# Kernel tuning notes

Hardware: AMD Instinct MI355X
Metric: run time of the kernel (lower is better)

## Reference

```python
import jax, jax.numpy as jnp
import numpy as np

EMBED_VOCAB = 16 * 1024 * 1024
EPS = 1e-5


def setup_inputs() -> dict:
    key = jax.random.key(0)
    ks = jax.random.split(key, 16)
    B = 65536
    state = jax.random.randint(ks[0], (B,), 0, 4, dtype=jnp.int32)
    counts = jax.random.randint(ks[1], (B,), 0, 200, dtype=jnp.int32)
    mp = jax.random.randint(ks[2], (B, 7, 7), 0, EMBED_VOCAB, dtype=jnp.int32)
    # learned parameters
    embed_table = jax.random.normal(ks[3], (EMBED_VOCAB, 8), dtype=jnp.float32)
    state_table = jax.random.normal(ks[4], (4, 32), dtype=jnp.float32)
    counts_table = jax.random.normal(ks[5], (200, 16), dtype=jnp.float32)
    d_in = 8 * 49 + 32 + 16  # 440
    W1 = jax.random.normal(ks[6], (256, d_in), dtype=jnp.float32) * (1.0 / np.sqrt(d_in))
    b1 = jnp.zeros((256,), dtype=jnp.float32)
    gamma = jnp.ones((256,), dtype=jnp.float32)
    beta = jnp.zeros((256,), dtype=jnp.float32)
    W2 = jax.random.normal(ks[7], (64, 256), dtype=jnp.float32) * (1.0 / np.sqrt(256))
    b2 = jnp.zeros((64,), dtype=jnp.float32)
    W3 = jax.random.normal(ks[8], (16, 64), dtype=jnp.float32) * (1.0 / np.sqrt(64))
    b3 = jnp.zeros((16,), dtype=jnp.float32)
    W4 = jax.random.normal(ks[9], (1, 16), dtype=jnp.float32) * 0.25
    b4 = jnp.zeros((1,), dtype=jnp.float32)
    return {
        "state": state, "counts": counts, "mp": mp,
        "embed_table": embed_table, "state_table": state_table, "counts_table": counts_table,
        "W1": W1, "b1": b1, "gamma": gamma, "beta": beta,
        "W2": W2, "b2": b2, "W3": W3, "b3": b3, "W4": W4, "b4": b4,
    }


def reference(state, counts, mp, embed_table, state_table, counts_table,
              W1, b1, gamma, beta, W2, b2, W3, b3, W4, b4):
    B = mp.shape[0]
    # gather embeddings
    x = embed_table[jnp.remainder(mp, EMBED_VOCAB)]      # [B,7,7,8]
    x = x.reshape(B, 49 * 8)                              # flatten dims 1..2 then last
    s = state_table[state]                                # [B,32]
    c = counts_table[counts]                              # [B,16]
    h = jnp.concatenate((s, c, x), axis=1)                # [B,440]
    # Linear 440->256
    h = h @ W1.T + b1
    # BatchNorm1d(256), training mode (batch statistics, biased variance)
    mu = jnp.mean(h, axis=0)
    var = jnp.mean((h - mu) ** 2, axis=0)
    h = (h - mu) * jax.lax.rsqrt(var + EPS) * gamma + beta
    # Linear 256->64 + ReLU
    h = jax.nn.relu(h @ W2.T + b2)
    # Linear 64->16 + ReLU
    h = jax.nn.relu(h @ W3.T + b3)
    # Linear 16->1
    out = h @ W4.T + b4                                   # [B,1]
    return out.reshape(B)
```

## Files before the change

### kernel.cpp

```cpp
#include <hip/hip_runtime.h>

typedef __attribute__((ext_vector_type(4))) float f32x4;
typedef __attribute__((ext_vector_type(8))) short bfrag;

#define NCH 256
#define BN_EPS 1e-5f

__device__ __forceinline__ unsigned short cvt_bf16(float f){
  unsigned u = __float_as_uint(f);
  u += 0x7FFFu + ((u >> 16) & 1u);
  return (unsigned short)(u >> 16);
}
__device__ __forceinline__ float bf16tof(unsigned short h){
  return __uint_as_float(((unsigned)h) << 16);
}
__device__ __forceinline__ void split2(const f32x4 va, const f32x4 vb, bfrag& hi, bfrag& lo){
  #pragma unroll
  for (int e = 0; e < 4; ++e){
    unsigned short h0 = cvt_bf16(va[e]);
    hi[e]   = (short)h0;
    lo[e]   = (short)cvt_bf16(va[e] - bf16tof(h0));
    unsigned short h1b = cvt_bf16(vb[e]);
    hi[4+e] = (short)h1b;
    lo[4+e] = (short)cvt_bf16(vb[e] - bf16tof(h1b));
  }
}

#define GLOAD_LDS16(gp, lp) \
  __builtin_amdgcn_global_load_lds((const __attribute__((address_space(1))) unsigned*)(gp), \
                                   (__attribute__((address_space(3))) unsigned*)(lp), 16, 0, 0)

__global__ void k_prep(const float* __restrict__ W1, const float* __restrict__ W2,
                       unsigned short* __restrict__ W1p, unsigned short* __restrict__ W2p,
                       float* __restrict__ gsum){
  int t = blockIdx.x * 256 + threadIdx.x;
  if (t < 14 * 8192){
    int e = t & 7, l = (t >> 3) & 63, c = (t >> 9) & 15, s = t >> 13;
    int chan = c * 16 + (l & 15);
    int k = s * 32 + (l >> 4) * 8 + e;
    float v = (k < 440) ? W1[chan * 440 + k] : 0.f;
    W1p[s * 8192 + c * 512 + l * 8 + e] = cvt_bf16(v);
  }
  if (t < 16384){
    int e = t & 7, l = (t >> 3) & 63, c = (t >> 9) & 3, s = t >> 11;
    int chan = c * 16 + (l & 15);
    int k = s * 32 + (l >> 4) * 8 + e;
    W2p[s * 2048 + c * 512 + l * 8 + e] = cvt_bf16(W2[chan * 256 + k]);
  }
  if (t < 512) gsum[t] = 0.f;
}

__device__ __forceinline__ void stage_w(const char* __restrict__ wsrc, char* smem,
                                        int S, int BUF, int w, int l){
  #pragma unroll
  for (int r = 0; r < 4; ++r)
    GLOAD_LDS16(wsrc + S * 16384 + (w * 4 + r) * 1024 + l * 16,
                smem + BUF * 16384 + (w * 4 + r) * 1024);
}

__global__ __launch_bounds__(256, 2) void k_gemm1(
    const int* __restrict__ state, const int* __restrict__ counts, const int* __restrict__ mp,
    const float* __restrict__ embed, const float* __restrict__ stab, const float* __restrict__ ctab,
    const unsigned short* __restrict__ W1p, const float* __restrict__ b1,
    unsigned short* __restrict__ h1b, float* __restrict__ gsum)
{
  __shared__ __align__(16) char smem[2 * 16384];
  __shared__ __align__(16) int  mp_lds[6272];
  __shared__ float wsum[4][256];
  __shared__ float wsq[4][256];

  const int tid = threadIdx.x;
  const int w  = tid >> 6;
  const int l  = tid & 63;
  const int lr = l & 15;
  const int g  = l >> 4;
  const int rowbase = blockIdx.x * 128 + w * 32;
  const int arow0 = rowbase + lr;
  const int arow1 = rowbase + 16 + lr;

  const int st0 = state[arow0] * 32, st1 = state[arow1] * 32;
  const int ct0 = counts[arow0] * 16, ct1 = counts[arow1] * 16;
  const char* wsrc = (const char*)W1p;

  {
    const char* mpsrc = (const char*)(mp + (size_t)blockIdx.x * 6272);
    #pragma unroll
    for (int it = 0; it < 7; ++it){
      int idx = it * 256 + tid;
      if (idx < 1568)
        GLOAD_LDS16(mpsrc + idx * 16, (char*)mp_lds + idx * 16);
    }
  }

  f32x4 xva[3][2], xvb[3][2];
  f32x4 acc0[16], acc1[16];
  #pragma unroll
  for (int i = 0; i < 16; ++i){ acc0[i] = (f32x4){0.f,0.f,0.f,0.f}; acc1[i] = acc0[i]; }

  #define ISSUE_X(S) do {                                            \
    const float *p0_, *p1_;                                          \
    if ((S) == 0){ p0_ = stab + st0 + g * 8; p1_ = stab + st1 + g * 8; } \
    else if ((S) == 1 && g < 2){                                     \
      p0_ = ctab + ct0 + g * 8; p1_ = ctab + ct1 + g * 8;            \
    } else {                                                         \
      int m_ = 4 * (S) + g - 6;                                      \
      m_ = m_ < 0 ? 0 : (m_ > 48 ? 48 : m_);                         \
      p0_ = embed + ((mp_lds[(w * 32 + lr) * 49 + m_]      & 0xFFFFFF) << 3); \
      p1_ = embed + ((mp_lds[(w * 32 + 16 + lr) * 49 + m_] & 0xFFFFFF) << 3); \
    }                                                                \
    xva[(S)%3][0] = *(const f32x4*)p0_;  xvb[(S)%3][0] = *(const f32x4*)(p0_ + 4); \
    xva[(S)%3][1] = *(const f32x4*)p1_;  xvb[(S)%3][1] = *(const f32x4*)(p1_ + 4); \
  } while(0)

  stage_w(wsrc, smem, 0, 0, w, l);
  ISSUE_X(0);
  asm volatile("s_waitcnt vmcnt(0)" ::: "memory");
  __builtin_amdgcn_sched_barrier(0);
  __builtin_amdgcn_s_barrier();
  ISSUE_X(1);
  asm volatile("" ::: "memory");
  __builtin_amdgcn_sched_barrier(0);

  bfrag ahi0, alo0, ahi1, alo1;

  #pragma unroll
  for (int s = 0; s < 14; ++s){
    if (s < 13) stage_w(wsrc, smem, s + 1, (s + 1) & 1, w, l);
    asm volatile("" ::: "memory");
    __builtin_amdgcn_sched_barrier(0);

    {
      f32x4 va0 = xva[s % 3][0], vb0 = xvb[s % 3][0];
      f32x4 va1 = xva[s % 3][1], vb1 = xvb[s % 3][1];
      if (s == 13 && g == 3){
        va0 = (f32x4){0.f,0.f,0.f,0.f}; vb0 = va0; va1 = va0; vb1 = va0;
      }
      split2(va0, vb0, ahi0, alo0);
      split2(va1, vb1, ahi1, alo1);
    }
    if (s < 12) ISSUE_X(s + 2);

    __builtin_amdgcn_sched_barrier(0);
    if (s <= 11)      asm volatile("s_waitcnt vmcnt(12)" ::: "memory");
    else if (s == 12) asm volatile("s_waitcnt vmcnt(8)"  ::: "memory");
    else              asm volatile("s_waitcnt vmcnt(0)"  ::: "memory");
    __builtin_amdgcn_sched_barrier(0);
    __builtin_amdgcn_s_barrier();

    {
      const char* base = smem + (s & 1) * 16384 + l * 16;
      #pragma unroll
      for (int c = 0; c < 16; ++c){
        const bfrag bhi = *(const bfrag*)(base + c * 1024);
        acc0[c] = __builtin_amdgcn_mfma_f32_16x16x32_bf16(ahi0, bhi, acc0[c], 0, 0, 0);
        acc0[c] = __builtin_amdgcn_mfma_f32_16x16x32_bf16(alo0, bhi, acc0[c], 0, 0, 0);
        acc1[c] = __builtin_amdgcn_mfma_f32_16x16x32_bf16(ahi1, bhi, acc1[c], 0, 0, 0);
        acc1[c] = __builtin_amdgcn_mfma_f32_16x16x32_bf16(alo1, bhi, acc1[c], 0, 0, 0);
      }
    }

    __builtin_amdgcn_s_barrier();
  }
  #undef ISSUE_X

  #pragma unroll
  for (int c = 0; c < 16; ++c){
    const int j = c * 16 + lr;
    const float bb = b1[j];
    float s = 0.f, q = 0.f;
    #pragma unroll
    for (int e = 0; e < 4; ++e){
      float h = acc0[c][e] + bb;
      s += h; q += h * h;
      h1b[(rowbase + g * 4 + e) * NCH + j] = cvt_bf16(h);
    }
    #pragma unroll
    for (int e = 0; e < 4; ++e){
      float h = acc1[c][e] + bb;
      s += h; q += h * h;
      h1b[(rowbase + 16 + g * 4 + e) * NCH + j] = cvt_bf16(h);
    }
    s += __shfl_xor(s, 16);  s += __shfl_xor(s, 32);
    q += __shfl_xor(q, 16);  q += __shfl_xor(q, 32);
    if (g == 0){ wsum[w][j] = s; wsq[w][j] = q; }
  }
  __syncthreads();
  {
    float s = wsum[0][tid] + wsum[1][tid] + wsum[2][tid] + wsum[3][tid];
    float q = wsq[0][tid]  + wsq[1][tid]  + wsq[2][tid]  + wsq[3][tid];
    atomicAdd(&gsum[tid], s);
    atomicAdd(&gsum[256 + tid], q);
  }
}

__global__ __launch_bounds__(256, 3) void k_tail(
    const unsigned short* __restrict__ h1b, const float* __restrict__ gsum,
    const float* __restrict__ gamma, const float* __restrict__ beta,
    const unsigned short* __restrict__ W2p,
    const float* __restrict__ b2, const float* __restrict__ W3, const float* __restrict__ b3,
    const float* __restrict__ W4, const float* __restrict__ b4,
    float* __restrict__ out)
{
  __shared__ float ssl[512];
  __shared__ __align__(16) short w2s[16384];
  __shared__ float h2l[4][16][65];

  const int tid = threadIdx.x;
  const int w  = tid >> 6;
  const int l  = tid & 63;
  const int lr = l & 15;
  const int g  = l >> 4;
  const int rowbase = blockIdx.x * 128 + w * 32;

  {
    float su = gsum[tid];
    float sq = gsum[256 + tid];
    float mu  = su * (1.f / 65536.f);
    float var = sq * (1.f / 65536.f) - mu * mu;
    float sc  = gamma[tid] * rsqrtf(var + BN_EPS);
    ssl[tid]       = sc;
    ssl[256 + tid] = beta[tid] - mu * sc;
  }
  #pragma unroll
  for (int it = 0; it < 8; ++it)
    GLOAD_LDS16((const char*)W2p + (it * 256 + tid) * 16, (char*)w2s + (it * 256 + tid) * 16);
  __syncthreads();

  const float b4v = b4[0];

  #pragma unroll
  for (int t = 0; t < 2; ++t){
    const int rowt = rowbase + t * 16;

    f32x4 acc[4];
    #pragma unroll
    for (int i = 0; i < 4; ++i) acc[i] = (f32x4){0.f, 0.f, 0.f, 0.f};

    #pragma unroll
    for (int s = 0; s < 8; ++s){
      const int kk = s * 32 + g * 8;
      bfrag hv = *(const bfrag*)(h1b + (rowt + lr) * 256 + kk);
      bfrag ahi, alo;
      #pragma unroll
      for (int e = 0; e < 8; ++e){
        float x = fmaf(bf16tof((unsigned short)hv[e]), ssl[kk + e], ssl[256 + kk + e]);
        unsigned short h0 = cvt_bf16(x);
        ahi[e] = (short)h0;
        alo[e] = (short)cvt_bf16(x - bf16tof(h0));
      }
      const char* base = (const char*)w2s + s * 4096 + l * 16;
      #pragma unroll
      for (int c = 0; c < 4; ++c){
        const bfrag bhi = *(const bfrag*)(base + c * 1024);
        acc[c] = __builtin_amdgcn_mfma_f32_16x16x32_bf16(ahi, bhi, acc[c], 0, 0, 0);
        acc[c] = __builtin_amdgcn_mfma_f32_16x16x32_bf16(alo, bhi, acc[c], 0, 0, 0);
      }
    }

    #pragma unroll
    for (int c = 0; c < 4; ++c){
      int j = c * 16 + lr;
      float bb = b2[j];
      #pragma unroll
      for (int e = 0; e < 4; ++e){
        float h = acc[c][e] + bb;
        h2l[w][g * 4 + e][j] = h > 0.f ? h : 0.f;
      }
    }

    float a3[4];
    #pragma unroll
    for (int t3 = 0; t3 < 4; ++t3) a3[t3] = b3[g * 4 + t3];
    #pragma unroll 4
    for (int k = 0; k < 64; ++k){
      float hv = h2l[w][lr][k];
      #pragma unroll
      for (int t3 = 0; t3 < 4; ++t3) a3[t3] += hv * W3[(g * 4 + t3) * 64 + k];
    }

    float p = 0.f;
    #pragma unroll
    for (int t3 = 0; t3 < 4; ++t3){
      float h = a3[t3] > 0.f ? a3[t3] : 0.f;
      p += h * W4[g * 4 + t3];
    }
    p += __shfl_xor(p, 16);
    p += __shfl_xor(p, 32);
    if (l < 16) out[rowt + lr] = p + b4v;
  }
}

extern "C" void kernel_launch(void* const* d_in, const int* in_sizes, int n_in,
                              void* d_out, int out_size, void* d_ws, size_t ws_size,
                              hipStream_t stream){
  const int*   state = (const int*)d_in[0];
  const int*   counts= (const int*)d_in[1];
  const int*   mp    = (const int*)d_in[2];
  const float* embed = (const float*)d_in[3];
  const float* stab  = (const float*)d_in[4];
  const float* ctab  = (const float*)d_in[5];
  const float* W1    = (const float*)d_in[6];
  const float* b1    = (const float*)d_in[7];
  const float* gamma = (const float*)d_in[8];
  const float* beta  = (const float*)d_in[9];
  const float* W2    = (const float*)d_in[10];
  const float* b2    = (const float*)d_in[11];
  const float* W3    = (const float*)d_in[12];
  const float* b3    = (const float*)d_in[13];
  const float* W4    = (const float*)d_in[14];
  const float* b4    = (const float*)d_in[15];
  float* out = (float*)d_out;

  char* ws = (char*)d_ws;
  unsigned short* h1bf = (unsigned short*)(ws);
  float* gsum          = (float*)(ws + 33554432);
  unsigned short* W1p  = (unsigned short*)(ws + 33558528);
  unsigned short* W2p  = (unsigned short*)(ws + 33787904);

  k_prep <<<448, 256, 0, stream>>>(W1, W2, W1p, W2p, gsum);
  k_gemm1<<<512, 256, 0, stream>>>(state, counts, mp, embed, stab, ctab,
                                   W1p, b1, h1bf, gsum);
  k_tail <<<512, 256, 0, stream>>>(h1bf, gsum, gamma, beta, W2p,
                                   b2, W3, b3, W4, b4, out);
}
```

Before: 117.4 us.

## Warp-specialize gemm1: producer waves gather and split embeddings into LDS for MFMA waves

Each gemm1 block now has 512 threads. Four producer waves gather the state, counts and embedding rows, split them into bf16 hi/lo pairs, and write them to a double-buffered, XOR-swizzled LDS area. Four consumer waves stage W1 and run the MFMAs on the A fragments read from LDS. The mp indices are read straight from global instead of being staged in LDS. The per-block stat reduction in LDS is replaced with per-wave atomics to gsum. The aim is to overlap random gather latency with the matrix work, at the cost of 64KB of LDS per block, more atomics, and a reliance on the barrier count matching between the two roles.

```diff
diff --git a/kernel.cpp b/kernel.cpp
--- a/kernel.cpp
+++ b/kernel.cpp
@@ -58,97 +58,117 @@
                 smem + BUF * 16384 + (w * 4 + r) * 1024);
 }
 
-__global__ __launch_bounds__(256, 2) void k_gemm1(
+__global__ __launch_bounds__(512, 2) void k_gemm1(
     const int* __restrict__ state, const int* __restrict__ counts, const int* __restrict__ mp,
     const float* __restrict__ embed, const float* __restrict__ stab, const float* __restrict__ ctab,
     const unsigned short* __restrict__ W1p, const float* __restrict__ b1,
     unsigned short* __restrict__ h1b, float* __restrict__ gsum)
 {
-  __shared__ __align__(16) char smem[2 * 16384];
-  __shared__ __align__(16) int  mp_lds[6272];
-  __shared__ float wsum[4][256];
-  __shared__ float wsq[4][256];
+  __shared__ __align__(16) char lds[65536];
 
   const int tid = threadIdx.x;
   const int w  = tid >> 6;
   const int l  = tid & 63;
-  const int lr = l & 15;
-  const int g  = l >> 4;
-  const int rowbase = blockIdx.x * 128 + w * 32;
-  const int arow0 = rowbase + lr;
-  const int arow1 = rowbase + 16 + lr;
-
-  const int st0 = state[arow0] * 32, st1 = state[arow1] * 32;
-  const int ct0 = counts[arow0] * 16, ct1 = counts[arow1] * 16;
   const char* wsrc = (const char*)W1p;
 
-  {
-    const char* mpsrc = (const char*)(mp + (size_t)blockIdx.x * 6272);
-    #pragma unroll
-    for (int it = 0; it < 7; ++it){
-      int idx = it * 256 + tid;
-      if (idx < 1568)
-        GLOAD_LDS16(mpsrc + idx * 16, (char*)mp_lds + idx * 16);
-    }
-  }
-
-  f32x4 xva[3][2], xvb[3][2];
-  f32x4 acc0[16], acc1[16];
-  #pragma unroll
-  for (int i = 0; i < 16; ++i){ acc0[i] = (f32x4){0.f,0.f,0.f,0.f}; acc1[i] = acc0[i]; }
-
-  #define ISSUE_X(S) do {                                            \
-    const float *p0_, *p1_;                                          \
-    if ((S) == 0){ p0_ = stab + st0 + g * 8; p1_ = stab + st1 + g * 8; } \
-    else if ((S) == 1 && g < 2){                                     \
-      p0_ = ctab + ct0 + g * 8; p1_ = ctab + ct1 + g * 8;            \
-    } else {                                                         \
-      int m_ = 4 * (S) + g - 6;                                      \
-      m_ = m_ < 0 ? 0 : (m_ > 48 ? 48 : m_);                         \
-      p0_ = embed + ((mp_lds[(w * 32 + lr) * 49 + m_]      & 0xFFFFFF) << 3); \
-      p1_ = embed + ((mp_lds[(w * 32 + 16 + lr) * 49 + m_] & 0xFFFFFF) << 3); \
-    }                                                                \
-    xva[(S)%3][0] = *(const f32x4*)p0_;  xvb[(S)%3][0] = *(const f32x4*)(p0_ + 4); \
-    xva[(S)%3][1] = *(const f32x4*)p1_;  xvb[(S)%3][1] = *(const f32x4*)(p1_ + 4); \
-  } while(0)
-
-  stage_w(wsrc, smem, 0, 0, w, l);
-  ISSUE_X(0);
-  asm volatile("s_waitcnt vmcnt(0)" ::: "memory");
-  __builtin_amdgcn_sched_barrier(0);
-  __builtin_amdgcn_s_barrier();
-  ISSUE_X(1);
-  asm volatile("" ::: "memory");
-  __builtin_amdgcn_sched_barrier(0);
-
-  bfrag ahi0, alo0, ahi1, alo1;
-
-  #pragma unroll
-  for (int s = 0; s < 14; ++s){
-    if (s < 13) stage_w(wsrc, smem, s + 1, (s + 1) & 1, w, l);
-    asm volatile("" ::: "memory");
-    __builtin_amdgcn_sched_barrier(0);
-
+  if (w >= 4){
+    const int q  = w - 4;
+    const int g  = l & 3;
+    const int rA = q * 32 + (l >> 2);
+    const int rB = rA + 16;
+    const int gA = blockIdx.x * 128 + rA;
+    const int gB = blockIdx.x * 128 + rB;
+
+    const int stA = state[gA] * 32,  stB = state[gB] * 32;
+    const int ctA = counts[gA] * 16, ctB = counts[gB] * 16;
+
+    int   mAv[14], mBv[14];
+    f32x4 pa[14][2], pb[14][2];
+
+    #define MCOL(S) ((S) == 1 ? (g >= 2 ? g - 2 : 0) \
+                              : (4*(S) + g - 6 > 48 ? 48 : 4*(S) + g - 6))
+
+    mAv[1] = mp[gA * 49 + MCOL(1)];  mBv[1] = mp[gB * 49 + MCOL(1)];
+    mAv[2] = mp[gA * 49 + MCOL(2)];  mBv[2] = mp[gB * 49 + MCOL(2)];
     {
-      f32x4 va0 = xva[s % 3][0], vb0 = xvb[s % 3][0];
-      f32x4 va1 = xva[s % 3][1], vb1 = xvb[s % 3][1];
-      if (s == 13 && g == 3){
-        va0 = (f32x4){0.f,0.f,0.f,0.f}; vb0 = va0; va1 = va0; vb1 = va0;
-      }
-      split2(va0, vb0, ahi0, alo0);
-      split2(va1, vb1, ahi1, alo1);
-    }
-    if (s < 12) ISSUE_X(s + 2);
-
-    __builtin_amdgcn_sched_barrier(0);
-    if (s <= 11)      asm volatile("s_waitcnt vmcnt(12)" ::: "memory");
-    else if (s == 12) asm volatile("s_waitcnt vmcnt(8)"  ::: "memory");
-    else              asm volatile("s_waitcnt vmcnt(0)"  ::: "memory");
-    __builtin_amdgcn_sched_barrier(0);
-    __builtin_amdgcn_s_barrier();
-
+      const float* aA = stab + stA + g * 8;
+      const float* aB = stab + stB + g * 8;
+      pa[0][0] = *(const f32x4*)aA; pb[0][0] = *(const f32x4*)(aA + 4);
+      pa[0][1] = *(const f32x4*)aB; pb[0][1] = *(const f32x4*)(aB + 4);
+    }
     {
-      const char* base = smem + (s & 1) * 16384 + l * 16;
+      const float* aA = (g < 2) ? (ctab + ctA + g * 8) : (embed + ((mAv[1] & 0xFFFFFF) << 3));
+      const float* aB = (g < 2) ? (ctab + ctB + g * 8) : (embed + ((mBv[1] & 0xFFFFFF) << 3));
+      pa[1][0] = *(const f32x4*)aA; pb[1][0] = *(const f32x4*)(aA + 4);
+      pa[1][1] = *(const f32x4*)aB; pb[1][1] = *(const f32x4*)(aB + 4);
+    }
+
+    #pragma unroll
+    for (int S = 0; S < 14; ++S){
+      if (S <= 10){
+        mAv[S+3] = mp[gA * 49 + MCOL(S+3)];
+        mBv[S+3] = mp[gB * 49 + MCOL(S+3)];
+      }
+      f32x4 a0 = pa[S][0], b0 = pb[S][0], a1 = pa[S][1], b1r = pb[S][1];
+      if (S == 13 && g == 3){
+        a0 = (f32x4){0.f,0.f,0.f,0.f}; b0 = a0; a1 = a0; b1r = a0;
+      }
+      bfrag hi0, lo0, hi1, lo1;
+      split2(a0, b0, hi0, lo0);
+      split2(a1, b1r, hi1, lo1);
+      {
+        char* slot = lds + 32768 + (S & 1) * 16384;
+        *(bfrag*)(slot + rA*128 + ((g*16)      ^ ((rA & 7) << 4))) = hi0;
+        *(bfrag*)(slot + rA*128 + ((64 + g*16) ^ ((rA & 7) << 4))) = lo0;
+        *(bfrag*)(slot + rB*128 + ((g*16)      ^ ((rB & 7) << 4))) = hi1;
+        *(bfrag*)(slot + rB*128 + ((64 + g*16) ^ ((rB & 7) << 4))) = lo1;
+      }
+      if (S <= 11){
+        const float* aA = embed + ((mAv[S+2] & 0xFFFFFF) << 3);
+        const float* aB = embed + ((mBv[S+2] & 0xFFFFFF) << 3);
+        pa[S+2][0] = *(const f32x4*)aA; pb[S+2][0] = *(const f32x4*)(aA + 4);
+        pa[S+2][1] = *(const f32x4*)aB; pb[S+2][1] = *(const f32x4*)(aB + 4);
+      }
+      __builtin_amdgcn_sched_barrier(0);
+      asm volatile("s_waitcnt lgkmcnt(0)" ::: "memory");
+      __builtin_amdgcn_sched_barrier(0);
+      __builtin_amdgcn_s_barrier();
+      __builtin_amdgcn_s_barrier();
+    }
+    #undef MCOL
+    return;
+
+  } else {
+    const int lr = l & 15;
+    const int g  = l >> 4;
+    const int rowbase = blockIdx.x * 128 + w * 32;
+    const int rl0 = w * 32 + lr, rl1 = rl0 + 16;
+
+    f32x4 acc0[16], acc1[16];
+    #pragma unroll
+    for (int i = 0; i < 16; ++i){ acc0[i] = (f32x4){0.f,0.f,0.f,0.f}; acc1[i] = acc0[i]; }
+
+    stage_w(wsrc, lds, 0, 0, w, l);
+
+    #pragma unroll
+    for (int S = 0; S < 14; ++S){
+      if (S < 13) stage_w(wsrc, lds, S + 1, (S + 1) & 1, w, l);
+
+      __builtin_amdgcn_sched_barrier(0);
+      if (S < 13) asm volatile("s_waitcnt vmcnt(4)" ::: "memory");
+      else        asm volatile("s_waitcnt vmcnt(0)" ::: "memory");
+      __builtin_amdgcn_sched_barrier(0);
+      __builtin_amdgcn_s_barrier();
+      asm volatile("" ::: "memory");
+      __builtin_amdgcn_sched_barrier(0);
+
+      const char* slot = lds + 32768 + (S & 1) * 16384;
+      const bfrag ahi0 = *(const bfrag*)(slot + rl0*128 + ((g*16)      ^ ((rl0 & 7) << 4)));
+      const bfrag alo0 = *(const bfrag*)(slot + rl0*128 + ((64 + g*16) ^ ((rl0 & 7) << 4)));
+      const bfrag ahi1 = *(const bfrag*)(slot + rl1*128 + ((g*16)      ^ ((rl1 & 7) << 4)));
+      const bfrag alo1 = *(const bfrag*)(slot + rl1*128 + ((64 + g*16) ^ ((rl1 & 7) << 4)));
+
+      const char* base = lds + (S & 1) * 16384 + l * 16;
       #pragma unroll
       for (int c = 0; c < 16; ++c){
         const bfrag bhi = *(const bfrag*)(base + c * 1024);
@@ -157,39 +177,33 @@
         acc1[c] = __builtin_amdgcn_mfma_f32_16x16x32_bf16(ahi1, bhi, acc1[c], 0, 0, 0);
         acc1[c] = __builtin_amdgcn_mfma_f32_16x16x32_bf16(alo1, bhi, acc1[c], 0, 0, 0);
       }
-    }
-
-    __builtin_amdgcn_s_barrier();
-  }
-  #undef ISSUE_X
-
-  #pragma unroll
-  for (int c = 0; c < 16; ++c){
-    const int j = c * 16 + lr;
-    const float bb = b1[j];
-    float s = 0.f, q = 0.f;
-    #pragma unroll
-    for (int e = 0; e < 4; ++e){
-      float h = acc0[c][e] + bb;
-      s += h; q += h * h;
-      h1b[(rowbase + g * 4 + e) * NCH + j] = cvt_bf16(h);
-    }
-    #pragma unroll
-    for (int e = 0; e < 4; ++e){
-      float h = acc1[c][e] + bb;
-      s += h; q += h * h;
-      h1b[(rowbase + 16 + g * 4 + e) * NCH + j] = cvt_bf16(h);
-    }
-    s += __shfl_xor(s, 16);  s += __shfl_xor(s, 32);
-    q += __shfl_xor(q, 16);  q += __shfl_xor(q, 32);
-    if (g == 0){ wsum[w][j] = s; wsq[w][j] = q; }
-  }
-  __syncthreads();
-  {
-    float s = wsum[0][tid] + wsum[1][tid] + wsum[2][tid] + wsum[3][tid];
-    float q = wsq[0][tid]  + wsq[1][tid]  + wsq[2][tid]  + wsq[3][tid];
-    atomicAdd(&gsum[tid], s);
-    atomicAdd(&gsum[256 + tid], q);
+      __builtin_amdgcn_s_barrier();
+    }
+
+    #pragma unroll
+    for (int c = 0; c < 16; ++c){
+      const int j = c * 16 + lr;
+      const float bb = b1[j];
+      float s = 0.f, qq = 0.f;
+      #pragma unroll
+      for (int e = 0; e < 4; ++e){
+        float h = acc0[c][e] + bb;
+        s += h; qq += h * h;
+        h1b[(rowbase + g * 4 + e) * NCH + j] = cvt_bf16(h);
+      }
+      #pragma unroll
+      for (int e = 0; e < 4; ++e){
+        float h = acc1[c][e] + bb;
+        s += h; qq += h * h;
+        h1b[(rowbase + 16 + g * 4 + e) * NCH + j] = cvt_bf16(h);
+      }
+      s  += __shfl_xor(s, 16);  s  += __shfl_xor(s, 32);
+      qq += __shfl_xor(qq, 16); qq += __shfl_xor(qq, 32);
+      if (g == 0){
+        atomicAdd(&gsum[j], s);
+        atomicAdd(&gsum[256 + j], qq);
+      }
+    }
   }
 }
 
@@ -318,7 +332,7 @@
   unsigned short* W2p  = (unsigned short*)(ws + 33787904);
 
   k_prep <<<448, 256, 0, stream>>>(W1, W2, W1p, W2p, gsum);
-  k_gemm1<<<512, 256, 0, stream>>>(state, counts, mp, embed, stab, ctab,
+  k_gemm1<<<512, 512, 0, stream>>>(state, counts, mp, embed, stab, ctab,
                                    W1p, b1, h1bf, gsum);
   k_tail <<<512, 256, 0, stream>>>(h1bf, gsum, gamma, beta, W2p,
                                    b2, W3, b3, W4, b4, out);
```

Measured after the change: 152.5 us. 1.3x slower.

## Fuse GEMM1 and tail via grid-wide barrier, keep activations in registers

Applied to the files above, without the earlier changes.

Merges the first GEMM and the BatchNorm/MLP tail into one persistent kernel. A global atomic counter acts as a grid barrier after the batch statistics are accumulated, so the 256-wide hidden activations stay in MFMA accumulators instead of being written to and re-read from a bf16 buffer in global memory. The MFMA operands are swapped so the accumulator layout feeds directly into the second GEMM's A fragments, and W2 is repacked to match. This removes a kernel launch and roughly 64 MB of HBM traffic plus bf16 rounding of h1. The cost is that all 512 blocks must be co-resident or the spin-wait deadlocks, and the barrier serialises the slowest block.

```diff
diff --git a/kernel.cpp b/kernel.cpp
--- a/kernel.cpp
+++ b/kernel.cpp
@@ -4,6 +4,7 @@
 typedef __attribute__((ext_vector_type(8))) short bfrag;
 
 #define NCH 256
+#define NBLK 512
 #define BN_EPS 1e-5f
 
 __device__ __forceinline__ unsigned short cvt_bf16(float f){
@@ -42,12 +43,12 @@
     W1p[s * 8192 + c * 512 + l * 8 + e] = cvt_bf16(v);
   }
   if (t < 16384){
-    int e = t & 7, l = (t >> 3) & 63, c = (t >> 9) & 3, s = t >> 11;
-    int chan = c * 16 + (l & 15);
-    int k = s * 32 + (l >> 4) * 8 + e;
-    W2p[s * 2048 + c * 512 + l * 8 + e] = cvt_bf16(W2[chan * 256 + k]);
-  }
-  if (t < 512) gsum[t] = 0.f;
+    int e = t & 7, l = (t >> 3) & 63, c2 = (t >> 9) & 3, s2 = t >> 11;
+    int j2 = c2 * 16 + (l & 15);
+    int ch = (2 * s2 + (e >> 2)) * 16 + ((l >> 4) << 2) + (e & 3);
+    W2p[t] = cvt_bf16(W2[j2 * 256 + ch]);
+  }
+  if (t < 516) gsum[t] = 0.f;
 }
 
 __device__ __forceinline__ void stage_w(const char* __restrict__ wsrc, char* smem,
@@ -58,16 +59,24 @@
                 smem + BUF * 16384 + (w * 4 + r) * 1024);
 }
 
-__global__ __launch_bounds__(256, 2) void k_gemm1(
+__global__ __launch_bounds__(256, 2) void k_fused(
     const int* __restrict__ state, const int* __restrict__ counts, const int* __restrict__ mp,
     const float* __restrict__ embed, const float* __restrict__ stab, const float* __restrict__ ctab,
     const unsigned short* __restrict__ W1p, const float* __restrict__ b1,
-    unsigned short* __restrict__ h1b, float* __restrict__ gsum)
+    const unsigned short* __restrict__ W2p, const float* __restrict__ b2,
+    const float* __restrict__ W3, const float* __restrict__ b3,
+    const float* __restrict__ W4, const float* __restrict__ b4,
+    const float* __restrict__ gamma, const float* __restrict__ beta,
+    float* __restrict__ gsum, float* __restrict__ out)
 {
-  __shared__ __align__(16) char smem[2 * 16384];
-  __shared__ __align__(16) int  mp_lds[6272];
-  __shared__ float wsum[4][256];
-  __shared__ float wsq[4][256];
+  __shared__ __align__(16) char lds[57856];
+  char*  smem   = lds;
+  int*   mp_lds = (int*)(lds + 32768);
+  float* wsum   = (float*)(lds + 32768);
+  float* wsq    = (float*)(lds + 36864);
+  float* ssl    = (float*)(lds + 32768);
+  float* h2l    = (float*)(lds + 34816);
+  unsigned* cnt = (unsigned*)(gsum + 512);
 
   const int tid = threadIdx.x;
   const int w  = tid >> 6;
@@ -151,143 +160,133 @@
       const char* base = smem + (s & 1) * 16384 + l * 16;
       #pragma unroll
       for (int c = 0; c < 16; ++c){
-        const bfrag bhi = *(const bfrag*)(base + c * 1024);
-        acc0[c] = __builtin_amdgcn_mfma_f32_16x16x32_bf16(ahi0, bhi, acc0[c], 0, 0, 0);
-        acc0[c] = __builtin_amdgcn_mfma_f32_16x16x32_bf16(alo0, bhi, acc0[c], 0, 0, 0);
-        acc1[c] = __builtin_amdgcn_mfma_f32_16x16x32_bf16(ahi1, bhi, acc1[c], 0, 0, 0);
-        acc1[c] = __builtin_amdgcn_mfma_f32_16x16x32_bf16(alo1, bhi, acc1[c], 0, 0, 0);
+        const bfrag whi = *(const bfrag*)(base + c * 1024);
+        acc0[c] = __builtin_amdgcn_mfma_f32_16x16x32_bf16(whi, ahi0, acc0[c], 0, 0, 0);
+        acc0[c] = __builtin_amdgcn_mfma_f32_16x16x32_bf16(whi, alo0, acc0[c], 0, 0, 0);
+        acc1[c] = __builtin_amdgcn_mfma_f32_16x16x32_bf16(whi, ahi1, acc1[c], 0, 0, 0);
+        acc1[c] = __builtin_amdgcn_mfma_f32_16x16x32_bf16(whi, alo1, acc1[c], 0, 0, 0);
       }
     }
-
     __builtin_amdgcn_s_barrier();
   }
   #undef ISSUE_X
 
   #pragma unroll
+  for (int it = 0; it < 8; ++it)
+    GLOAD_LDS16((const char*)W2p + (it * 256 + tid) * 16, lds + (it * 256 + tid) * 16);
+
+  #pragma unroll
   for (int c = 0; c < 16; ++c){
-    const int j = c * 16 + lr;
-    const float bb = b1[j];
-    float s = 0.f, q = 0.f;
+    f32x4 bb = *(const f32x4*)(b1 + c * 16 + g * 4);
+    acc0[c] += bb;
+    acc1[c] += bb;
     #pragma unroll
     for (int e = 0; e < 4; ++e){
-      float h = acc0[c][e] + bb;
-      s += h; q += h * h;
-      h1b[(rowbase + g * 4 + e) * NCH + j] = cvt_bf16(h);
+      float v0 = acc0[c][e], v1 = acc1[c][e];
+      float s = v0 + v1, q = v0 * v0 + v1 * v1;
+      s += __shfl_xor(s, 1); q += __shfl_xor(q, 1);
+      s += __shfl_xor(s, 2); q += __shfl_xor(q, 2);
+      s += __shfl_xor(s, 4); q += __shfl_xor(q, 4);
+      s += __shfl_xor(s, 8); q += __shfl_xor(q, 8);
+      if (lr == 0){
+        int ch = c * 16 + g * 4 + e;
+        wsum[w * 256 + ch] = s;
+        wsq [w * 256 + ch] = q;
+      }
     }
-    #pragma unroll
-    for (int e = 0; e < 4; ++e){
-      float h = acc1[c][e] + bb;
-      s += h; q += h * h;
-      h1b[(rowbase + 16 + g * 4 + e) * NCH + j] = cvt_bf16(h);
-    }
-    s += __shfl_xor(s, 16);  s += __shfl_xor(s, 32);
-    q += __shfl_xor(q, 16);  q += __shfl_xor(q, 32);
-    if (g == 0){ wsum[w][j] = s; wsq[w][j] = q; }
   }
   __syncthreads();
   {
-    float s = wsum[0][tid] + wsum[1][tid] + wsum[2][tid] + wsum[3][tid];
-    float q = wsq[0][tid]  + wsq[1][tid]  + wsq[2][tid]  + wsq[3][tid];
+    float s = wsum[tid] + wsum[256 + tid] + wsum[512 + tid] + wsum[768 + tid];
+    float q = wsq[tid]  + wsq[256 + tid]  + wsq[512 + tid]  + wsq[768 + tid];
     atomicAdd(&gsum[tid], s);
     atomicAdd(&gsum[256 + tid], q);
   }
-}
-
-__global__ __launch_bounds__(256, 3) void k_tail(
-    const unsigned short* __restrict__ h1b, const float* __restrict__ gsum,
-    const float* __restrict__ gamma, const float* __restrict__ beta,
-    const unsigned short* __restrict__ W2p,
-    const float* __restrict__ b2, const float* __restrict__ W3, const float* __restrict__ b3,
-    const float* __restrict__ W4, const float* __restrict__ b4,
-    float* __restrict__ out)
-{
-  __shared__ float ssl[512];
-  __shared__ __align__(16) short w2s[16384];
-  __shared__ float h2l[4][16][65];
-
-  const int tid = threadIdx.x;
-  const int w  = tid >> 6;
-  const int l  = tid & 63;
-  const int lr = l & 15;
-  const int g  = l >> 4;
-  const int rowbase = blockIdx.x * 128 + w * 32;
+
+  __threadfence();
+  __syncthreads();
+  if (tid == 0){
+    __hip_atomic_fetch_add(cnt, 1u, __ATOMIC_ACQ_REL, __HIP_MEMORY_SCOPE_AGENT);
+    while (__hip_atomic_load(cnt, __ATOMIC_ACQUIRE, __HIP_MEMORY_SCOPE_AGENT) < NBLK)
+      __builtin_amdgcn_s_sleep(2);
+  }
+  __syncthreads();
 
   {
-    float su = gsum[tid];
-    float sq = gsum[256 + tid];
+    float su = __hip_atomic_load(&gsum[tid],       __ATOMIC_RELAXED, __HIP_MEMORY_SCOPE_AGENT);
+    float sq = __hip_atomic_load(&gsum[256 + tid], __ATOMIC_RELAXED, __HIP_MEMORY_SCOPE_AGENT);
     float mu  = su * (1.f / 65536.f);
     float var = sq * (1.f / 65536.f) - mu * mu;
     float sc  = gamma[tid] * rsqrtf(var + BN_EPS);
     ssl[tid]       = sc;
     ssl[256 + tid] = beta[tid] - mu * sc;
   }
-  #pragma unroll
-  for (int it = 0; it < 8; ++it)
-    GLOAD_LDS16((const char*)W2p + (it * 256 + tid) * 16, (char*)w2s + (it * 256 + tid) * 16);
   __syncthreads();
 
   const float b4v = b4[0];
 
-  #pragma unroll
-  for (int t = 0; t < 2; ++t){
-    const int rowt = rowbase + t * 16;
-
-    f32x4 acc[4];
-    #pragma unroll
-    for (int i = 0; i < 4; ++i) acc[i] = (f32x4){0.f, 0.f, 0.f, 0.f};
-
-    #pragma unroll
-    for (int s = 0; s < 8; ++s){
-      const int kk = s * 32 + g * 8;
-      bfrag hv = *(const bfrag*)(h1b + (rowt + lr) * 256 + kk);
-      bfrag ahi, alo;
-      #pragma unroll
-      for (int e = 0; e < 8; ++e){
-        float x = fmaf(bf16tof((unsigned short)hv[e]), ssl[kk + e], ssl[256 + kk + e]);
-        unsigned short h0 = cvt_bf16(x);
-        ahi[e] = (short)h0;
-        alo[e] = (short)cvt_bf16(x - bf16tof(h0));
-      }
-      const char* base = (const char*)w2s + s * 4096 + l * 16;
-      #pragma unroll
-      for (int c = 0; c < 4; ++c){
-        const bfrag bhi = *(const bfrag*)(base + c * 1024);
-        acc[c] = __builtin_amdgcn_mfma_f32_16x16x32_bf16(ahi, bhi, acc[c], 0, 0, 0);
-        acc[c] = __builtin_amdgcn_mfma_f32_16x16x32_bf16(alo, bhi, acc[c], 0, 0, 0);
-      }
-    }
-
-    #pragma unroll
-    for (int c = 0; c < 4; ++c){
-      int j = c * 16 + lr;
-      float bb = b2[j];
-      #pragma unroll
-      for (int e = 0; e < 4; ++e){
-        float h = acc[c][e] + bb;
-        h2l[w][g * 4 + e][j] = h > 0.f ? h : 0.f;
-      }
-    }
-
-    float a3[4];
-    #pragma unroll
-    for (int t3 = 0; t3 < 4; ++t3) a3[t3] = b3[g * 4 + t3];
-    #pragma unroll 4
-    for (int k = 0; k < 64; ++k){
-      float hv = h2l[w][lr][k];
-      #pragma unroll
-      for (int t3 = 0; t3 < 4; ++t3) a3[t3] += hv * W3[(g * 4 + t3) * 64 + k];
-    }
-
-    float p = 0.f;
-    #pragma unroll
-    for (int t3 = 0; t3 < 4; ++t3){
-      float h = a3[t3] > 0.f ? a3[t3] : 0.f;
-      p += h * W4[g * 4 + t3];
-    }
-    p += __shfl_xor(p, 16);
-    p += __shfl_xor(p, 32);
-    if (l < 16) out[rowt + lr] = p + b4v;
-  }
+#define TAIL_TILE(ACC, TOFF) do {                                                  \
+    f32x4 acc2[4];                                                                 \
+    acc2[0] = (f32x4){0.f,0.f,0.f,0.f};                                            \
+    acc2[1] = acc2[0]; acc2[2] = acc2[0]; acc2[3] = acc2[0];                       \
+    _Pragma("unroll")                                                              \
+    for (int s2 = 0; s2 < 8; ++s2){                                                \
+      bfrag ahi, alo;                                                              \
+      _Pragma("unroll")                                                            \
+      for (int hh = 0; hh < 2; ++hh){                                              \
+        const int c = 2 * s2 + hh;                                                 \
+        f32x4 sc = *(const f32x4*)(ssl + c * 16 + g * 4);                          \
+        f32x4 sh = *(const f32x4*)(ssl + 256 + c * 16 + g * 4);                    \
+        _Pragma("unroll")                                                          \
+        for (int e = 0; e < 4; ++e){                                               \
+          float x = ACC[c][e] * sc[e] + sh[e];                                     \
+          unsigned short h0 = cvt_bf16(x);                                         \
+          ahi[hh * 4 + e] = (short)h0;                                             \
+          alo[hh * 4 + e] = (short)cvt_bf16(x - bf16tof(h0));                      \
+        }                                                                          \
+      }                                                                            \
+      const char* wb = smem + s2 * 4096 + l * 16;                                  \
+      _Pragma("unroll")                                                            \
+      for (int c2 = 0; c2 < 4; ++c2){                                              \
+        const bfrag bh = *(const bfrag*)(wb + c2 * 1024);                          \
+        acc2[c2] = __builtin_amdgcn_mfma_f32_16x16x32_bf16(ahi, bh, acc2[c2],0,0,0); \
+        acc2[c2] = __builtin_amdgcn_mfma_f32_16x16x32_bf16(alo, bh, acc2[c2],0,0,0); \
+      }                                                                            \
+    }                                                                              \
+    float* hw = h2l + w * 1040;                                                    \
+    _Pragma("unroll")                                                              \
+    for (int c2 = 0; c2 < 4; ++c2){                                                \
+      const int j = c2 * 16 + lr;                                                  \
+      const float bb2 = b2[j];                                                     \
+      _Pragma("unroll")                                                            \
+      for (int e = 0; e < 4; ++e){                                                 \
+        float h = acc2[c2][e] + bb2;                                               \
+        hw[(g * 4 + e) * 65 + j] = h > 0.f ? h : 0.f;                              \
+      }                                                                            \
+    }                                                                              \
+    float a3[4];                                                                   \
+    _Pragma("unroll")                                                              \
+    for (int t3 = 0; t3 < 4; ++t3) a3[t3] = b3[g * 4 + t3];                        \
+    _Pragma("unroll 4")                                                            \
+    for (int k = 0; k < 64; ++k){                                                  \
+      float hv = hw[lr * 65 + k];                                                  \
+      _Pragma("unroll")                                                            \
+      for (int t3 = 0; t3 < 4; ++t3) a3[t3] += hv * W3[(g * 4 + t3) * 64 + k];     \
+    }                                                                              \
+    float p = 0.f;                                                                 \
+    _Pragma("unroll")                                                              \
+    for (int t3 = 0; t3 < 4; ++t3){                                                \
+      float h = a3[t3] > 0.f ? a3[t3] : 0.f;                                       \
+      p += h * W4[g * 4 + t3];                                                     \
+    }                                                                              \
+    p += __shfl_xor(p, 16);                                                        \
+    p += __shfl_xor(p, 32);                                                        \
+    if (l < 16) out[rowbase + (TOFF) + lr] = p + b4v;                              \
+  } while (0)
+
+  TAIL_TILE(acc0, 0);
+  TAIL_TILE(acc1, 16);
+#undef TAIL_TILE
 }
 
 extern "C" void kernel_launch(void* const* d_in, const int* in_sizes, int n_in,
@@ -312,14 +311,12 @@
   float* out = (float*)d_out;
 
   char* ws = (char*)d_ws;
-  unsigned short* h1bf = (unsigned short*)(ws);
-  float* gsum          = (float*)(ws + 33554432);
-  unsigned short* W1p  = (unsigned short*)(ws + 33558528);
-  unsigned short* W2p  = (unsigned short*)(ws + 33787904);
+  float* gsum          = (float*)(ws);
+  unsigned short* W1p  = (unsigned short*)(ws + 4096);
+  unsigned short* W2p  = (unsigned short*)(ws + 4096 + 229376);
 
   k_prep <<<448, 256, 0, stream>>>(W1, W2, W1p, W2p, gsum);
-  k_gemm1<<<512, 256, 0, stream>>>(state, counts, mp, embed, stab, ctab,
-                                   W1p, b1, h1bf, gsum);
-  k_tail <<<512, 256, 0, stream>>>(h1bf, gsum, gamma, beta, W2p,
-                                   b2, W3, b3, W4, b4, out);
-}
+  k_fused<<<NBLK, 256, 0, stream>>>(state, counts, mp, embed, stab, ctab,
+                                    W1p, b1, W2p, b2, W3, b3, W4, b4,
+                                    gamma, beta, gsum, out);
+}
```

New measurement: 174.4 us. 48.5% more time.

## Halve rows per block in GEMM1 and reuse LDS to raise occupancy

Applied to the files above, without the earlier changes.

Each wave of the first GEMM kernel now handles 16 rows instead of 32, so each block covers 64 rows and the grid doubles to 1024 blocks. The BN partial-sum scratch now reuses the weight staging buffer, and launch bounds go from 2 to 3 blocks per SM. Lower register and LDS use should allow more resident waves to hide the latency of the random embedding gathers. In exchange, each staged W1 tile is reused by half as many rows, so weight traffic per row doubles, and more blocks issue atomic adds to the global BN sums.

```diff
diff --git a/kernel.cpp b/kernel.cpp
--- a/kernel.cpp
+++ b/kernel.cpp
@@ -58,58 +58,54 @@
                 smem + BUF * 16384 + (w * 4 + r) * 1024);
 }
 
-__global__ __launch_bounds__(256, 2) void k_gemm1(
+__global__ __launch_bounds__(256, 3) void k_gemm1(
     const int* __restrict__ state, const int* __restrict__ counts, const int* __restrict__ mp,
     const float* __restrict__ embed, const float* __restrict__ stab, const float* __restrict__ ctab,
     const unsigned short* __restrict__ W1p, const float* __restrict__ b1,
     unsigned short* __restrict__ h1b, float* __restrict__ gsum)
 {
   __shared__ __align__(16) char smem[2 * 16384];
-  __shared__ __align__(16) int  mp_lds[6272];
-  __shared__ float wsum[4][256];
-  __shared__ float wsq[4][256];
+  __shared__ __align__(16) int  mp_lds[3136];
+  float* wsum = (float*)smem;
+  float* wsq  = (float*)(smem + 4096);
 
   const int tid = threadIdx.x;
   const int w  = tid >> 6;
   const int l  = tid & 63;
   const int lr = l & 15;
   const int g  = l >> 4;
-  const int rowbase = blockIdx.x * 128 + w * 32;
+  const int rowbase = blockIdx.x * 64 + w * 16;
   const int arow0 = rowbase + lr;
-  const int arow1 = rowbase + 16 + lr;
-
-  const int st0 = state[arow0] * 32, st1 = state[arow1] * 32;
-  const int ct0 = counts[arow0] * 16, ct1 = counts[arow1] * 16;
+
+  const int st0 = state[arow0] * 32;
+  const int ct0 = counts[arow0] * 16;
   const char* wsrc = (const char*)W1p;
 
   {
-    const char* mpsrc = (const char*)(mp + (size_t)blockIdx.x * 6272);
-    #pragma unroll
-    for (int it = 0; it < 7; ++it){
+    const char* mpsrc = (const char*)(mp + (size_t)blockIdx.x * 3136);
+    #pragma unroll
+    for (int it = 0; it < 4; ++it){
       int idx = it * 256 + tid;
-      if (idx < 1568)
+      if (idx < 784)
         GLOAD_LDS16(mpsrc + idx * 16, (char*)mp_lds + idx * 16);
     }
   }
 
-  f32x4 xva[3][2], xvb[3][2];
-  f32x4 acc0[16], acc1[16];
-  #pragma unroll
-  for (int i = 0; i < 16; ++i){ acc0[i] = (f32x4){0.f,0.f,0.f,0.f}; acc1[i] = acc0[i]; }
+  f32x4 xva[3], xvb[3];
+  f32x4 acc0[16];
+  #pragma unroll
+  for (int i = 0; i < 16; ++i) acc0[i] = (f32x4){0.f,0.f,0.f,0.f};
 
   #define ISSUE_X(S) do {                                            \
-    const float *p0_, *p1_;                                          \
-    if ((S) == 0){ p0_ = stab + st0 + g * 8; p1_ = stab + st1 + g * 8; } \
-    else if ((S) == 1 && g < 2){                                     \
-      p0_ = ctab + ct0 + g * 8; p1_ = ctab + ct1 + g * 8;            \
-    } else {                                                         \
+    const float *p0_;                                                \
+    if ((S) == 0){ p0_ = stab + st0 + g * 8; }                       \
+    else if ((S) == 1 && g < 2){ p0_ = ctab + ct0 + g * 8; }         \
+    else {                                                           \
       int m_ = 4 * (S) + g - 6;                                      \
       m_ = m_ < 0 ? 0 : (m_ > 48 ? 48 : m_);                         \
-      p0_ = embed + ((mp_lds[(w * 32 + lr) * 49 + m_]      & 0xFFFFFF) << 3); \
-      p1_ = embed + ((mp_lds[(w * 32 + 16 + lr) * 49 + m_] & 0xFFFFFF) << 3); \
+      p0_ = embed + ((mp_lds[(w * 16 + lr) * 49 + m_] & 0xFFFFFF) << 3); \
     }                                                                \
-    xva[(S)%3][0] = *(const f32x4*)p0_;  xvb[(S)%3][0] = *(const f32x4*)(p0_ + 4); \
-    xva[(S)%3][1] = *(const f32x4*)p1_;  xvb[(S)%3][1] = *(const f32x4*)(p1_ + 4); \
+    xva[(S)%3] = *(const f32x4*)p0_;  xvb[(S)%3] = *(const f32x4*)(p0_ + 4); \
   } while(0)
 
   stage_w(wsrc, smem, 0, 0, w, l);
@@ -121,7 +117,7 @@
   asm volatile("" ::: "memory");
   __builtin_amdgcn_sched_barrier(0);
 
-  bfrag ahi0, alo0, ahi1, alo1;
+  bfrag ahi0, alo0;
 
   #pragma unroll
   for (int s = 0; s < 14; ++s){
@@ -130,20 +126,18 @@
     __builtin_amdgcn_sched_barrier(0);
 
     {
-      f32x4 va0 = xva[s % 3][0], vb0 = xvb[s % 3][0];
-      f32x4 va1 = xva[s % 3][1], vb1 = xvb[s % 3][1];
+      f32x4 va0 = xva[s % 3], vb0 = xvb[s % 3];
       if (s == 13 && g == 3){
-        va0 = (f32x4){0.f,0.f,0.f,0.f}; vb0 = va0; va1 = va0; vb1 = va0;
+        va0 = (f32x4){0.f,0.f,0.f,0.f}; vb0 = va0;
       }
       split2(va0, vb0, ahi0, alo0);
-      split2(va1, vb1, ahi1, alo1);
     }
     if (s < 12) ISSUE_X(s + 2);
 
     __builtin_amdgcn_sched_barrier(0);
-    if (s <= 11)      asm volatile("s_waitcnt vmcnt(12)" ::: "memory");
-    else if (s == 12) asm volatile("s_waitcnt vmcnt(8)"  ::: "memory");
-    else              asm volatile("s_waitcnt vmcnt(0)"  ::: "memory");
+    if (s <= 11)      asm volatile("s_waitcnt vmcnt(8)" ::: "memory");
+    else if (s == 12) asm volatile("s_waitcnt vmcnt(6)" ::: "memory");
+    else              asm volatile("s_waitcnt vmcnt(0)" ::: "memory");
     __builtin_amdgcn_sched_barrier(0);
     __builtin_amdgcn_s_barrier();
 
@@ -154,8 +148,6 @@
         const bfrag bhi = *(const bfrag*)(base + c * 1024);
         acc0[c] = __builtin_amdgcn_mfma_f32_16x16x32_bf16(ahi0, bhi, acc0[c], 0, 0, 0);
         acc0[c] = __builtin_amdgcn_mfma_f32_16x16x32_bf16(alo0, bhi, acc0[c], 0, 0, 0);
-        acc1[c] = __builtin_amdgcn_mfma_f32_16x16x32_bf16(ahi1, bhi, acc1[c], 0, 0, 0);
-        acc1[c] = __builtin_amdgcn_mfma_f32_16x16x32_bf16(alo1, bhi, acc1[c], 0, 0, 0);
       }
     }
 
@@ -174,20 +166,14 @@
       s += h; q += h * h;
       h1b[(rowbase + g * 4 + e) * NCH + j] = cvt_bf16(h);
     }
-    #pragma unroll
-    for (int e = 0; e < 4; ++e){
-      float h = acc1[c][e] + bb;
-      s += h; q += h * h;
-      h1b[(rowbase + 16 + g * 4 + e) * NCH + j] = cvt_bf16(h);
-    }
     s += __shfl_xor(s, 16);  s += __shfl_xor(s, 32);
     q += __shfl_xor(q, 16);  q += __shfl_xor(q, 32);
-    if (g == 0){ wsum[w][j] = s; wsq[w][j] = q; }
+    if (g == 0){ wsum[w * 256 + j] = s; wsq[w * 256 + j] = q; }
   }
   __syncthreads();
   {
-    float s = wsum[0][tid] + wsum[1][tid] + wsum[2][tid] + wsum[3][tid];
-    float q = wsq[0][tid]  + wsq[1][tid]  + wsq[2][tid]  + wsq[3][tid];
+    float s = wsum[tid] + wsum[256 + tid] + wsum[512 + tid] + wsum[768 + tid];
+    float q = wsq[tid]  + wsq[256 + tid]  + wsq[512 + tid]  + wsq[768 + tid];
     atomicAdd(&gsum[tid], s);
     atomicAdd(&gsum[256 + tid], q);
   }
@@ -318,8 +304,8 @@
   unsigned short* W2p  = (unsigned short*)(ws + 33787904);
 
   k_prep <<<448, 256, 0, stream>>>(W1, W2, W1p, W2p, gsum);
-  k_gemm1<<<512, 256, 0, stream>>>(state, counts, mp, embed, stab, ctab,
-                                   W1p, b1, h1bf, gsum);
+  k_gemm1<<<1024, 256, 0, stream>>>(state, counts, mp, embed, stab, ctab,
+                                    W1p, b1, h1bf, gsum);
   k_tail <<<512, 256, 0, stream>>>(h1bf, gsum, gamma, beta, W2p,
                                    b2, W3, b3, W4, b4, out);
 }
```

Measured after the change: 124.0 us. 1.06x slower.
